# Optimization experiments

Measured on AMD Instinct MI355X. Metric: run time of the kernel, lower is better.

The kernel has to match this reference:

```python
import jax, jax.numpy as jnp
import numpy as np

N_ATOMS = 100000
N_EDGES = 200000  # paired: edge 2i and 2i+1 are reverses of each other
N_MOLS = 4096
D_V, D_E, D_H = 133, 14, 512
DEPTH = 3
BN_EPS = 1e-5


def setup_inputs() -> dict:
    key = jax.random.key(0)
    ks = jax.random.split(key, 10)
    V = jax.random.normal(ks[0], (N_ATOMS, D_V), dtype=jnp.float32)
    E = jax.random.normal(ks[1], (N_EDGES, D_E), dtype=jnp.float32)
    # paired directed edges: (src,dst) at 2i, (dst,src) at 2i+1 -> rev index is i^1
    half = N_EDGES // 2
    s = jax.random.randint(ks[2], (half,), 0, N_ATOMS, dtype=jnp.int32)
    d = jax.random.randint(ks[3], (half,), 0, N_ATOMS, dtype=jnp.int32)
    edge_src = jnp.stack([s, d], axis=1).reshape(-1)
    edge_dst = jnp.stack([d, s], axis=1).reshape(-1)
    batch = jnp.sort(jax.random.randint(ks[4], (N_ATOMS,), 0, N_MOLS, dtype=jnp.int32))
    sc = 0.02
    W_i = jax.random.normal(ks[5], (D_V + D_E, D_H), dtype=jnp.float32) * sc
    W_h = jax.random.normal(ks[6], (D_H, D_H), dtype=jnp.float32) * sc
    W_o = jax.random.normal(ks[7], (D_V + D_H, D_H), dtype=jnp.float32) * sc
    b_o = jnp.zeros((D_H,), dtype=jnp.float32)
    gamma = jnp.ones((D_H,), dtype=jnp.float32)
    beta = jnp.zeros((D_H,), dtype=jnp.float32)
    return {"V": V, "E": E, "edge_src": edge_src, "edge_dst": edge_dst,
            "batch": batch, "W_i": W_i, "W_h": W_h, "W_o": W_o, "b_o": b_o,
            "gamma": gamma, "beta": beta}


def reference(V, E, edge_src, edge_dst, batch, W_i, W_h, W_o, b_o, gamma, beta):
    n_atoms = V.shape[0]
    n_edges = E.shape[0]
    rev = jnp.arange(n_edges, dtype=jnp.int32) ^ 1  # reverse-bond index

    # --- BondMessagePassing (chemprop v2) ---
    # initialize: H_0 = W_i([V[src] ; E]), H = relu(H_0)
    H0 = jnp.concatenate([V[edge_src], E], axis=1) @ W_i  # [n_edges, d_h]
    H = jax.nn.relu(H0)
    for _ in range(DEPTH - 1):
        # message: sum of incoming edge states at dst node, gathered at src,
        # minus the reverse edge's own state
        M_node = jax.ops.segment_sum(H, edge_dst, num_segments=n_atoms)
        M = M_node[edge_src] - H[rev]
        # update: H = relu(H_0 + W_h(M)) (dropout = 0)
        H = jax.nn.relu(H0 + M @ W_h)
    # finalize: aggregate edges to nodes, H_v = relu(W_o([V ; M_v]))
    M_v = jax.ops.segment_sum(H, edge_dst, num_segments=n_atoms)
    H_v = jax.nn.relu(jnp.concatenate([V, M_v], axis=1) @ W_o + b_o)  # [n_atoms, d_h]

    # --- MeanAggregation over batch ids ---
    sums = jax.ops.segment_sum(H_v, batch, num_segments=N_MOLS)
    counts = jax.ops.segment_sum(jnp.ones((n_atoms,), H_v.dtype), batch, num_segments=N_MOLS)
    h_mol = sums / jnp.maximum(counts, 1.0)[:, None]  # [n_mols, d_h]

    # --- BatchNorm1d (training mode: batch statistics, biased variance) ---
    mu = h_mol.mean(axis=0)
    var = h_mol.var(axis=0)
    return (h_mol - mu) * jax.lax.rsqrt(var + BN_EPS) * gamma + beta
```

## Files before the change

kernel.cpp:

```cpp
#include <hip/hip_runtime.h>

typedef _Float16 f16;
typedef _Float16 half8 __attribute__((ext_vector_type(8)));
typedef _Float16 half4v __attribute__((ext_vector_type(4)));
typedef float f32x4 __attribute__((ext_vector_type(4)));

#define N_ATOMS 100000
#define N_EDGES 200000
#define N_MOLS  4096
#define D_V 133
#define D_E 14
#define D_H 512
#define KC  672
#define KSE 21
#define LDA 40

__global__ void wt_build_swz(const float* __restrict__ W1, int r1,
                             const float* __restrict__ W2, int r2,
                             f16* __restrict__ WtS) {
    int gid = blockIdx.x * blockDim.x + threadIdx.x;
    if (gid >= D_H * KC) return;
    int n = gid / KC;
    int k = gid - n * KC;
    float x = 0.f;
    if (k < r1) x = W1[k * D_H + n];
    else if (k < r1 + r2) x = W2[(k - r1) * D_H + n];
    const int dst = ((((n >> 4) * KSE + (k >> 5)) << 6) + (((k >> 3) & 3) << 4) + (n & 15)) * 8 + (k & 7);
    WtS[dst] = (f16)x;
}

__global__ void csr_hist(const int* __restrict__ edst, int* __restrict__ cnt) {
    int e = blockIdx.x * blockDim.x + threadIdx.x;
    if (e < N_EDGES) atomicAdd(&cnt[edst[e]], 1);
}

__global__ __launch_bounds__(1024) void csr_scan(const int* __restrict__ cnt,
                                                 int* __restrict__ off, int* __restrict__ pos) {
    __shared__ int sums[1024];
    const int tid = threadIdx.x;
    const int lo = tid * 100;
    int s = 0;
    if (lo < N_ATOMS) {
        const int4* c4 = reinterpret_cast<const int4*>(cnt + lo);
        #pragma unroll
        for (int i = 0; i < 25; ++i) { int4 v = c4[i]; s += v.x + v.y + v.z + v.w; }
    }
    sums[tid] = s;
    __syncthreads();
    for (int d = 1; d < 1024; d <<= 1) {
        int v = (tid >= d) ? sums[tid - d] : 0;
        __syncthreads();
        sums[tid] += v;
        __syncthreads();
    }
    int run = sums[tid] - s;
    if (lo < N_ATOMS) {
        const int4* c4 = reinterpret_cast<const int4*>(cnt + lo);
        for (int i = 0; i < 25; ++i) {
            int4 v = c4[i];
            const int b = lo + i * 4;
            off[b]     = run; pos[b]     = run; run += v.x;
            off[b + 1] = run; pos[b + 1] = run; run += v.y;
            off[b + 2] = run; pos[b + 2] = run; run += v.z;
            off[b + 3] = run; pos[b + 3] = run; run += v.w;
        }
    }
    if (tid == 1023) off[N_ATOMS] = run;
}

__global__ void csr_scatter(const int* __restrict__ edst, int* __restrict__ pos,
                            int* __restrict__ eid) {
    int e = blockIdx.x * blockDim.x + threadIdx.x;
    if (e < N_EDGES) {
        int idx = atomicAdd(&pos[edst[e]], 1);
        eid[idx] = e;
    }
}

template<bool F16M>
__global__ __launch_bounds__(512) void seg_csr(
    const f16* __restrict__ H, const int* __restrict__ off, const int* __restrict__ eid,
    void* __restrict__ MnOut, float* __restrict__ Msc)
{
    const int n = blockIdx.x * 8 + (threadIdx.x >> 6);
    const int lane = threadIdx.x & 63;
    const int j0 = off[n], j1 = off[n + 1];
    float acc[8];
    #pragma unroll
    for (int k = 0; k < 8; ++k) acc[k] = 0.f;
    int e_cur = (j0 < j1) ? eid[j0] : 0;
    for (int j = j0; j < j1; ++j) {
        const int e_nxt = (j + 1 < j1) ? eid[j + 1] : 0;
        const half8 h = *reinterpret_cast<const half8*>(&H[e_cur * D_H + lane * 8]);
        #pragma unroll
        for (int k = 0; k < 8; ++k) acc[k] += (float)h[k];
        e_cur = e_nxt;
    }
    if (F16M) {
        half8 o;
        #pragma unroll
        for (int k = 0; k < 8; ++k) o[k] = (f16)acc[k];
        *reinterpret_cast<half8*>(&((f16*)MnOut)[n * D_H + lane * 8]) = o;
    } else {
        float m = 0.f;
        #pragma unroll
        for (int k = 0; k < 8; ++k) m = fmaxf(m, fabsf(acc[k]));
        m = fmaxf(m, __shfl_xor(m, 1));
        m = fmaxf(m, __shfl_xor(m, 2));
        m = fmaxf(m, 1e-20f);
        const float s = m * (1.f / 127.f);
        const float inv_s = 127.f / m;
        if ((lane & 3) == 0) Msc[n * 16 + (lane >> 2)] = s;
        int q[8];
        #pragma unroll
        for (int k = 0; k < 8; ++k) q[k] = __float2int_rn(acc[k] * inv_s);
        uint2 o;
        o.x = (q[0] & 0xff) | ((q[1] & 0xff) << 8) | ((q[2] & 0xff) << 16) | ((unsigned)(q[3] & 0xff) << 24);
        o.y = (q[4] & 0xff) | ((q[5] & 0xff) << 8) | ((q[6] & 0xff) << 16) | ((unsigned)(q[7] & 0xff) << 24);
        *reinterpret_cast<uint2*>(&((unsigned int*)MnOut)[n * 128 + lane * 2]) = o;
    }
}

template<bool F16M>
__global__ __launch_bounds__(512) void gemm_pass(
    const float* __restrict__ V, const float* __restrict__ E,
    const int* __restrict__ esrc, const void* __restrict__ Mn,
    const float* __restrict__ Msc,
    f16* __restrict__ Ha, const f16* __restrict__ WtS, int ks_begin)
{
    __shared__ __align__(16) f16 Al[64 * LDA];
    const int tid = threadIdx.x;
    const int rowblk = blockIdx.x << 6;
    const int srow = tid >> 3;
    const int skk  = (tid & 7) << 2;
    const int e_s  = rowblk + srow;
    const int sv   = esrc[e_s];
    const int rev  = e_s ^ 1;
    const int lane = tid & 63;
    const int quad = lane >> 4;
    const int m16  = lane & 15;
    const int colbase = (tid >> 6) << 6;
    const int cb0 = (tid >> 6) << 2;
    const f16* WtL = WtS + lane * 8;

    f32x4 acc[4][4];
    #pragma unroll
    for (int a = 0; a < 4; ++a)
    #pragma unroll
    for (int b = 0; b < 4; ++b)
    #pragma unroll
    for (int r = 0; r < 4; ++r) acc[a][b][r] = 0.f;

    char4 pq; float ps; half4v pm; half4v ph; float pv[4];
    auto issue = [&](int ks) {
        const int k0 = ks << 5;
        if (k0 < D_H) {
            if (F16M) {
                pm = *reinterpret_cast<const half4v*>(&((const f16*)Mn)[sv * D_H + k0 + skk]);
            } else {
                pq = *reinterpret_cast<const char4*>(&((const char*)Mn)[sv * D_H + k0 + skk]);
                ps = Msc[sv * 16 + (k0 >> 5)];
            }
            ph = *reinterpret_cast<const half4v*>(&Ha[rev * D_H + k0 + skk]);
        } else {
            #pragma unroll
            for (int j = 0; j < 4; ++j) {
                const int kk = k0 + skk + j - D_H;
                float x = 0.f;
                if (kk < D_V) x = V[sv * D_V + kk];
                else if (kk < D_V + D_E) x = E[e_s * D_E + (kk - D_V)];
                pv[j] = x;
            }
        }
    };

    issue(ks_begin);
    for (int ks = ks_begin; ks < KSE; ++ks) {
        const int k0 = ks << 5;
        half4v w;
        if (k0 < D_H) {
            if (F16M) {
                w = pm - ph;
            } else {
                w[0] = (f16)((float)pq.x * ps - (float)ph[0]);
                w[1] = (f16)((float)pq.y * ps - (float)ph[1]);
                w[2] = (f16)((float)pq.z * ps - (float)ph[2]);
                w[3] = (f16)((float)pq.w * ps - (float)ph[3]);
            }
        } else {
            w[0] = (f16)pv[0]; w[1] = (f16)pv[1]; w[2] = (f16)pv[2]; w[3] = (f16)pv[3];
        }
        __syncthreads();
        *reinterpret_cast<half4v*>(&Al[srow * LDA + skk]) = w;
        __syncthreads();
        if (ks + 1 < KSE) issue(ks + 1);
        half8 af[4];
        #pragma unroll
        for (int rt = 0; rt < 4; ++rt)
            af[rt] = *reinterpret_cast<const half8*>(&Al[(rt * 16 + m16) * LDA + quad * 8]);
        #pragma unroll
        for (int ct = 0; ct < 4; ++ct) {
            const half8 bf = *reinterpret_cast<const half8*>(&WtL[(((cb0 + ct) * KSE + ks) << 9)]);
            #pragma unroll
            for (int rt = 0; rt < 4; ++rt)
                acc[rt][ct] = __builtin_amdgcn_mfma_f32_16x16x32_f16(af[rt], bf, acc[rt][ct], 0, 0, 0);
        }
    }

    #pragma unroll
    for (int rt = 0; rt < 4; ++rt)
    #pragma unroll
    for (int ct = 0; ct < 4; ++ct)
    #pragma unroll
    for (int r = 0; r < 4; ++r) {
        const int row = rowblk + rt * 16 + quad * 4 + r;
        const int col = colbase + ct * 16 + m16;
        Ha[row * D_H + col] = (f16)fmaxf(acc[rt][ct][r], 0.f);
    }
}

template<bool F16M>
__global__ __launch_bounds__(512) void gemm_out(
    const float* __restrict__ V, const void* __restrict__ Mn,
    const float* __restrict__ Msc, const float* __restrict__ bo,
    const f16* __restrict__ WtS, f16* __restrict__ Hv)
{
    __shared__ __align__(16) f16 Al[64 * LDA];
    __shared__ float bo_s[D_H];
    const int tid = threadIdx.x;
    const int rowblk = blockIdx.x << 6;
    bo_s[tid] = bo[tid];
    const int srow = tid >> 3;
    const int skk  = (tid & 7) << 2;
    const int arow = min(rowblk + srow, N_ATOMS - 1);
    const int lane = tid & 63;
    const int quad = lane >> 4;
    const int m16  = lane & 15;
    const int colbase = (tid >> 6) << 6;
    const int cb0 = (tid >> 6) << 2;
    const f16* WtL = WtS + lane * 8;

    f32x4 acc[4][4];
    #pragma unroll
    for (int a = 0; a < 4; ++a)
    #pragma unroll
    for (int b = 0; b < 4; ++b)
    #pragma unroll
    for (int r = 0; r < 4; ++r) acc[a][b][r] = 0.f;

    char4 pq; float ps; half4v pm; float pv[4];
    auto issue = [&](int ks) {
        const int k0 = ks << 5;
        if (k0 < D_H) {
            if (F16M) {
                pm = *reinterpret_cast<const half4v*>(&((const f16*)Mn)[arow * D_H + k0 + skk]);
            } else {
                pq = *reinterpret_cast<const char4*>(&((const char*)Mn)[arow * D_H + k0 + skk]);
                ps = Msc[arow * 16 + (k0 >> 5)];
            }
        } else {
            #pragma unroll
            for (int j = 0; j < 4; ++j) {
                const int kk = k0 + skk + j - D_H;
                pv[j] = (kk < D_V) ? V[arow * D_V + kk] : 0.f;
            }
        }
    };

    issue(0);
    for (int ks = 0; ks < KSE; ++ks) {
        const int k0 = ks << 5;
        half4v w;
        if (k0 < D_H) {
            if (F16M) {
                w = pm;
            } else {
                w[0] = (f16)((float)pq.x * ps);
                w[1] = (f16)((float)pq.y * ps);
                w[2] = (f16)((float)pq.z * ps);
                w[3] = (f16)((float)pq.w * ps);
            }
        } else {
            w[0] = (f16)pv[0]; w[1] = (f16)pv[1]; w[2] = (f16)pv[2]; w[3] = (f16)pv[3];
        }
        __syncthreads();
        *reinterpret_cast<half4v*>(&Al[srow * LDA + skk]) = w;
        __syncthreads();
        if (ks + 1 < KSE) issue(ks + 1);
        half8 af[4];
        #pragma unroll
        for (int rt = 0; rt < 4; ++rt)
            af[rt] = *reinterpret_cast<const half8*>(&Al[(rt * 16 + m16) * LDA + quad * 8]);
        #pragma unroll
        for (int ct = 0; ct < 4; ++ct) {
            const half8 bf = *reinterpret_cast<const half8*>(&WtL[(((cb0 + ct) * KSE + ks) << 9)]);
            #pragma unroll
            for (int rt = 0; rt < 4; ++rt)
                acc[rt][ct] = __builtin_amdgcn_mfma_f32_16x16x32_f16(af[rt], bf, acc[rt][ct], 0, 0, 0);
        }
    }

    #pragma unroll
    for (int rt = 0; rt < 4; ++rt)
    #pragma unroll
    for (int ct = 0; ct < 4; ++ct)
    #pragma unroll
    for (int r = 0; r < 4; ++r) {
        const int row = rowblk + rt * 16 + quad * 4 + r;
        if (row < N_ATOMS) {
            const int col = colbase + ct * 16 + m16;
            Hv[row * D_H + col] = (f16)fmaxf(acc[rt][ct][r] + bo_s[col], 0.f);
        }
    }
}

__global__ __launch_bounds__(512) void mol_mean(
    const f16* __restrict__ Hv, const int* __restrict__ batch, float* __restrict__ mean)
{
    const int m = blockIdx.x;
    __shared__ int sh[2];
    if (threadIdx.x == 0) {
        int lo = 0, hi = N_ATOMS;
        while (lo < hi) { int mid = (lo + hi) >> 1; if (batch[mid] < m) lo = mid + 1; else hi = mid; }
        sh[0] = lo;
        int lo2 = lo; hi = N_ATOMS;
        while (lo2 < hi) { int mid = (lo2 + hi) >> 1; if (batch[mid] < m + 1) lo2 = mid + 1; else hi = mid; }
        sh[1] = lo2;
    }
    __syncthreads();
    const int a0 = sh[0], a1 = sh[1];
    float acc = 0.f;
    for (int a = a0; a < a1; ++a) acc += (float)Hv[(size_t)a * D_H + threadIdx.x];
    mean[m * D_H + threadIdx.x] = acc / (float)max(a1 - a0, 1);
}

__global__ __launch_bounds__(256) void bn_stats(
    const float* __restrict__ mean_in, const float* __restrict__ gamma,
    const float* __restrict__ beta, float* __restrict__ An, float* __restrict__ Bn)
{
    const int n = blockIdx.x;
    const int tid = threadIdx.x;
    float s = 0.f, s2 = 0.f;
    for (int m = tid; m < N_MOLS; m += 256) {
        float h = mean_in[m * D_H + n];
        s += h; s2 += h * h;
    }
    for (int off = 32; off > 0; off >>= 1) {
        s  += __shfl_down(s, off);
        s2 += __shfl_down(s2, off);
    }
    __shared__ float sh[8];
    const int wave = tid >> 6, lane = tid & 63;
    if (lane == 0) { sh[wave] = s; sh[4 + wave] = s2; }
    __syncthreads();
    if (tid == 0) {
        float S  = sh[0] + sh[1] + sh[2] + sh[3];
        float S2 = sh[4] + sh[5] + sh[6] + sh[7];
        float mu = S / (float)N_MOLS;
        float var = fmaxf(S2 / (float)N_MOLS - mu * mu, 0.f);
        float sc = rsqrtf(var + 1e-5f) * gamma[n];
        An[n] = sc;
        Bn[n] = beta[n] - mu * sc;
    }
}

__global__ void bn_apply(const float* __restrict__ mean_in,
                         const float* __restrict__ An, const float* __restrict__ Bn,
                         float* __restrict__ out)
{
    int gid = blockIdx.x * blockDim.x + threadIdx.x;
    int n = gid & 511;
    out[gid] = mean_in[gid] * An[n] + Bn[n];
}

extern "C" void kernel_launch(void* const* d_in, const int* in_sizes, int n_in,
                              void* d_out, int out_size, void* d_ws, size_t ws_size,
                              hipStream_t stream)
{
    (void)in_sizes; (void)n_in; (void)out_size;
    const float* V     = (const float*)d_in[0];
    const float* E     = (const float*)d_in[1];
    const int*   esrc  = (const int*)d_in[2];
    const int*   edst  = (const int*)d_in[3];
    const int*   batch = (const int*)d_in[4];
    const float* Wi    = (const float*)d_in[5];
    const float* Wh    = (const float*)d_in[6];
    const float* Wo    = (const float*)d_in[7];
    const float* bo    = (const float*)d_in[8];
    const float* gam   = (const float*)d_in[9];
    const float* bet   = (const float*)d_in[10];
    float* out = (float*)d_out;

    char* ws = (char*)d_ws;
    f16*   WtC  = (f16*)(ws + 0);
    f16*   WtO  = (f16*)(ws + 688128);
    int*   off  = (int*)(ws + 1376256);
    int*   eid  = (int*)(ws + 1776384);
    int*   cnt  = (int*)(ws + 2576384);
    float* An   = (float*)(ws + 2992768);
    float* Bn   = (float*)(ws + 2994816);
    f16*   Ha   = (f16*)(ws + 2996864);
    void*  Mn   = (void*)(ws + 207796864);
    float* Msc  = (float*)(ws + 258996864);
    f16*   Hv   = Ha;
    float* mean = out;

    const bool f16m = ws_size >= 310196864ULL;

    wt_build_swz<<<(D_H * KC + 255) / 256, 256, 0, stream>>>(Wh, D_H, Wi, D_V + D_E, WtC);
    wt_build_swz<<<(D_H * KC + 255) / 256, 256, 0, stream>>>(Wo + D_V * D_H, D_H, Wo, D_V, WtO);

    hipMemsetAsync(cnt, 0, 400000, stream);
    csr_hist<<<(N_EDGES + 511) / 512, 512, 0, stream>>>(edst, cnt);
    csr_scan<<<1, 1024, 0, stream>>>(cnt, off, cnt);
    csr_scatter<<<(N_EDGES + 511) / 512, 512, 0, stream>>>(edst, cnt, eid);

    if (f16m) {
        gemm_pass<true><<<N_EDGES / 64, 512, 0, stream>>>(V, E, esrc, Mn, Msc, Ha, WtC, 16);
        for (int it = 0; it < 2; ++it) {
            seg_csr<true><<<N_ATOMS / 8, 512, 0, stream>>>(Ha, off, eid, Mn, Msc);
            gemm_pass<true><<<N_EDGES / 64, 512, 0, stream>>>(V, E, esrc, Mn, Msc, Ha, WtC, 0);
        }
        seg_csr<true><<<N_ATOMS / 8, 512, 0, stream>>>(Ha, off, eid, Mn, Msc);
        gemm_out<true><<<(N_ATOMS + 63) / 64, 512, 0, stream>>>(V, Mn, Msc, bo, WtO, Hv);
    } else {
        gemm_pass<false><<<N_EDGES / 64, 512, 0, stream>>>(V, E, esrc, Mn, Msc, Ha, WtC, 16);
        for (int it = 0; it < 2; ++it) {
            seg_csr<false><<<N_ATOMS / 8, 512, 0, stream>>>(Ha, off, eid, Mn, Msc);
            gemm_pass<false><<<N_EDGES / 64, 512, 0, stream>>>(V, E, esrc, Mn, Msc, Ha, WtC, 0);
        }
        seg_csr<false><<<N_ATOMS / 8, 512, 0, stream>>>(Ha, off, eid, Mn, Msc);
        gemm_out<false><<<(N_ATOMS + 63) / 64, 512, 0, stream>>>(V, Mn, Msc, bo, WtO, Hv);
    }

    mol_mean<<<N_MOLS, 512, 0, stream>>>(Hv, batch, mean);
    bn_stats<<<D_H, 256, 0, stream>>>(mean, gam, bet, An, Bn);
    bn_apply<<<(N_MOLS * D_H) / 256, 256, 0, stream>>>(mean, An, Bn, out);
}
```

Measured before the change: 1.334 ms.

## Double-buffer LDS A tile in output GEMM with deeper prefetch

The atom-level output GEMM now keeps two LDS buffers for the A tile. Each step stages the next k-slice into the idle buffer while MFMAs read the current one, so only one barrier per step is needed instead of two. Global loads are issued two slices ahead through two alternating register sets. This costs extra registers and LDS, and it only touches one of several kernels.

Measured after the change: 1.251 ms (median of 2 runs). 1.07x faster.

```diff
diff --git a/kernel.cpp b/kernel.cpp
--- a/kernel.cpp
+++ b/kernel.cpp
@@ -225,7 +225,7 @@
     const float* __restrict__ Msc, const float* __restrict__ bo,
     const f16* __restrict__ WtS, f16* __restrict__ Hv)
 {
-    __shared__ __align__(16) f16 Al[64 * LDA];
+    __shared__ __align__(16) f16 Al[2][64 * LDA];
     __shared__ float bo_s[D_H];
     const int tid = threadIdx.x;
     const int rowblk = blockIdx.x << 6;
@@ -248,57 +248,91 @@
     #pragma unroll
     for (int r = 0; r < 4; ++r) acc[a][b][r] = 0.f;
 
-    char4 pq; float ps; half4v pm; float pv[4];
-    auto issue = [&](int ks) {
-        const int k0 = ks << 5;
-        if (k0 < D_H) {
-            if (F16M) {
-                pm = *reinterpret_cast<const half4v*>(&((const f16*)Mn)[arow * D_H + k0 + skk]);
-            } else {
-                pq = *reinterpret_cast<const char4*>(&((const char*)Mn)[arow * D_H + k0 + skk]);
-                ps = Msc[arow * 16 + (k0 >> 5)];
-            }
-        } else {
-            #pragma unroll
-            for (int j = 0; j < 4; ++j) {
-                const int kk = k0 + skk + j - D_H;
-                pv[j] = (kk < D_V) ? V[arow * D_V + kk] : 0.f;
-            }
-        }
-    };
-
-    issue(0);
-    for (int ks = 0; ks < KSE; ++ks) {
-        const int k0 = ks << 5;
+    char4 pq0, pq1; float ps0, ps1;
+    half4v pm0, pm1;
+    float pv0[4], pv1[4];
+
+#define GO_ISSUE(S, KSV) do {                                                        \
+    const int ks_i_ = (KSV);                                                         \
+    if (ks_i_ < KSE) {                                                               \
+        const int k0_ = ks_i_ << 5;                                                  \
+        if (k0_ < D_H) {                                                             \
+            if (F16M) {                                                              \
+                pm##S = *reinterpret_cast<const half4v*>(&((const f16*)Mn)[arow * D_H + k0_ + skk]); \
+            } else {                                                                 \
+                pq##S = *reinterpret_cast<const char4*>(&((const char*)Mn)[arow * D_H + k0_ + skk]); \
+                ps##S = Msc[arow * 16 + (k0_ >> 5)];                                 \
+            }                                                                        \
+        } else {                                                                     \
+            const int kb_ = k0_ + skk - D_H;                                         \
+            pv##S[0] = (kb_ + 0 < D_V) ? V[arow * D_V + kb_ + 0] : 0.f;              \
+            pv##S[1] = (kb_ + 1 < D_V) ? V[arow * D_V + kb_ + 1] : 0.f;              \
+            pv##S[2] = (kb_ + 2 < D_V) ? V[arow * D_V + kb_ + 2] : 0.f;              \
+            pv##S[3] = (kb_ + 3 < D_V) ? V[arow * D_V + kb_ + 3] : 0.f;              \
+        }                                                                            \
+    }                                                                                \
+} while (0)
+
+#define GO_MAKEW(S, KSV, W) do {                                                     \
+    const int k0_ = (KSV) << 5;                                                      \
+    if (k0_ < D_H) {                                                                 \
+        if (F16M) { W = pm##S; }                                                     \
+        else {                                                                       \
+            W[0] = (f16)((float)pq##S.x * ps##S);                                    \
+            W[1] = (f16)((float)pq##S.y * ps##S);                                    \
+            W[2] = (f16)((float)pq##S.z * ps##S);                                    \
+            W[3] = (f16)((float)pq##S.w * ps##S);                                    \
+        }                                                                            \
+    } else {                                                                         \
+        W[0] = (f16)pv##S[0]; W[1] = (f16)pv##S[1];                                  \
+        W[2] = (f16)pv##S[2]; W[3] = (f16)pv##S[3];                                  \
+    }                                                                                \
+} while (0)
+
+#define GO_MFMA(KSV, CUR) do {                                                       \
+    half8 af[4];                                                                     \
+    _Pragma("unroll")                                                                \
+    for (int rt = 0; rt < 4; ++rt)                                                   \
+        af[rt] = *reinterpret_cast<const half8*>(&Al[CUR][(rt * 16 + m16) * LDA + quad * 8]); \
+    _Pragma("unroll")                                                                \
+    for (int ct = 0; ct < 4; ++ct) {                                                 \
+        const half8 bf = *reinterpret_cast<const half8*>(&WtL[(((cb0 + ct) * KSE + (KSV)) << 9)]); \
+        _Pragma("unroll")                                                            \
+        for (int rt = 0; rt < 4; ++rt)                                               \
+            acc[rt][ct] = __builtin_amdgcn_mfma_f32_16x16x32_f16(af[rt], bf, acc[rt][ct], 0, 0, 0); \
+    }                                                                                \
+} while (0)
+
+    GO_ISSUE(0, 0);
+    GO_ISSUE(1, 1);
+    {
         half4v w;
-        if (k0 < D_H) {
-            if (F16M) {
-                w = pm;
-            } else {
-                w[0] = (f16)((float)pq.x * ps);
-                w[1] = (f16)((float)pq.y * ps);
-                w[2] = (f16)((float)pq.z * ps);
-                w[3] = (f16)((float)pq.w * ps);
-            }
-        } else {
-            w[0] = (f16)pv[0]; w[1] = (f16)pv[1]; w[2] = (f16)pv[2]; w[3] = (f16)pv[3];
-        }
+        GO_MAKEW(0, 0, w);
+        *reinterpret_cast<half4v*>(&Al[0][srow * LDA + skk]) = w;
+        GO_ISSUE(0, 2);
+    }
+    __syncthreads();
+
+    #pragma unroll 2
+    for (int i = 0; i < KSE - 1; ++i) {
+        const int ks = i;
+        const int cur = i & 1;
+        {
+            half4v w;
+            if ((i + 1) & 1) { GO_MAKEW(1, ks + 1, w); }
+            else             { GO_MAKEW(0, ks + 1, w); }
+            *reinterpret_cast<half4v*>(&Al[cur ^ 1][srow * LDA + skk]) = w;
+            if ((i + 1) & 1) { GO_ISSUE(1, ks + 3); }
+            else             { GO_ISSUE(0, ks + 3); }
+        }
+        GO_MFMA(ks, cur);
         __syncthreads();
-        *reinterpret_cast<half4v*>(&Al[srow * LDA + skk]) = w;
-        __syncthreads();
-        if (ks + 1 < KSE) issue(ks + 1);
-        half8 af[4];
-        #pragma unroll
-        for (int rt = 0; rt < 4; ++rt)
-            af[rt] = *reinterpret_cast<const half8*>(&Al[(rt * 16 + m16) * LDA + quad * 8]);
-        #pragma unroll
-        for (int ct = 0; ct < 4; ++ct) {
-            const half8 bf = *reinterpret_cast<const half8*>(&WtL[(((cb0 + ct) * KSE + ks) << 9)]);
-            #pragma unroll
-            for (int rt = 0; rt < 4; ++rt)
-                acc[rt][ct] = __builtin_amdgcn_mfma_f32_16x16x32_f16(af[rt], bf, acc[rt][ct], 0, 0, 0);
-        }
-    }
+    }
+    GO_MFMA(KSE - 1, (KSE - 1) & 1);
+
+#undef GO_ISSUE
+#undef GO_MAKEW
+#undef GO_MFMA
 
     #pragma unroll
     for (int rt = 0; rt < 4; ++rt)
```
